# Optimization experiments

Hardware: AMD Instinct MI355X
Metric: run time of the kernel (lower is better)

Reference implementation:

```python
import jax, jax.numpy as jnp
import numpy as np

S, N, MSA_DIM, PAIR_DIM, D, H = 8, 256, 256, 128, 32, 8
EPS = 1e-5


def layer_norm(x, w, b):
    mu = jnp.mean(x, axis=-1, keepdims=True)
    var = jnp.mean((x - mu) ** 2, axis=-1, keepdims=True)
    return (x - mu) * jax.lax.rsqrt(var + EPS) * w + b


def setup_inputs() -> dict:
    key = jax.random.key(0)
    ks = jax.random.split(key, 8)
    def rnd(k, shape, scale=1.0):
        return jax.random.normal(k, shape, jnp.float32) * scale
    return {
        "msa_rep": rnd(ks[0], (S, N, MSA_DIM)),
        "pair_rep": rnd(ks[1], (N, N, PAIR_DIM)),
        "ln_w": jnp.ones((MSA_DIM,), jnp.float32),
        "ln_b": jnp.zeros((MSA_DIM,), jnp.float32),
        "w_qkv": rnd(ks[2], (MSA_DIM, 3 * H * D), 0.02),
        "ln_pair_w": jnp.ones((PAIR_DIM,), jnp.float32),
        "ln_pair_b": jnp.zeros((PAIR_DIM,), jnp.float32),
        "w_b": rnd(ks[3], (PAIR_DIM, H), 0.02),
        "w_g": rnd(ks[4], (MSA_DIM, H * D), 0.02),
        "w_out": rnd(ks[5], (H * D, MSA_DIM), 0.02),
        "b_out": jnp.zeros((MSA_DIM,), jnp.float32),
    }


def reference(msa_rep, pair_rep, ln_w, ln_b, w_qkv, ln_pair_w, ln_pair_b,
              w_b, w_g, w_out, b_out):
    s, n, _ = msa_rep.shape
    x = layer_norm(msa_rep, ln_w, ln_b)                      # [s, n, msa_dim]
    qkv = x @ w_qkv                                          # [s, n, 3*h*d]
    # chunk(3, dim=-1) then view(..., d, h): d outer, h inner
    q, k, v = [t.reshape(s, n, D, H) for t in jnp.split(qkv, 3, axis=-1)]
    # pair bias: LN + linear -> [n, n, h], broadcast to [1, i, j, 1, h]
    b = layer_norm(pair_rep, ln_pair_w, ln_pair_b) @ w_b     # [n, n, h]
    g = jax.nn.sigmoid(x @ w_g).reshape(s, n, D, H)          # gate [s, n, d, h]
    # NOTE: logits keep the d axis (no contraction): einsum 'sidh,sjdh->sijdh'
    scores = (q[:, :, None, :, :] * k[:, None, :, :, :]) * (D ** -0.5) \
             + b[None, :, :, None, :]                        # [s, i, j, d, h]
    a = jax.nn.softmax(scores, axis=2)                       # softmax over j
    out = g * jnp.einsum('sijdh,sjdh->sidh', a, v)           # [s, n, d, h]
    return out.reshape(s, n, D * H) @ w_out + b_out          # [s, n, msa_dim]
```

## Files before the change

### kernel.cpp

```cpp
#include <hip/hip_runtime.h>
#include <math.h>

#define S_DIM 8
#define N_RES 256
#define MSA_DIM 256
#define PAIR_DIM 128
#define D_DIM 32
#define H_DIM 8
#define M_ROWS (S_DIM * N_RES)
#define QKV_N (3 * H_DIM * D_DIM)
#define HD (H_DIM * D_DIM)
#define LOG2E 1.4426950408889634f

#define DPP_ADD(x, ctrl, rmask)                                                \
    x += __int_as_float(__builtin_amdgcn_update_dpp(                           \
        0, __float_as_int(x), (ctrl), (rmask), 0xf, true))

__device__ __forceinline__ float wave_sum63(float x) {
    DPP_ADD(x, 0x111, 0xf);
    DPP_ADD(x, 0x112, 0xf);
    DPP_ADD(x, 0x114, 0xf);
    DPP_ADD(x, 0x118, 0xf);
    DPP_ADD(x, 0x142, 0xa);
    DPP_ADD(x, 0x143, 0xc);
    return x;
}

__device__ __forceinline__ float quad_sum(float x) {
    x += __int_as_float(__builtin_amdgcn_update_dpp(
        0, __float_as_int(x), 0xB1, 0xf, 0xf, true));
    x += __int_as_float(__builtin_amdgcn_update_dpp(
        0, __float_as_int(x), 0x4E, 0xf, 0xf, true));
    return x;
}

__global__ __launch_bounds__(256) void ln_msa_kernel(
    const float* __restrict__ msa, const float* __restrict__ w,
    const float* __restrict__ b, float* __restrict__ x)
{
    int row = blockIdx.x;
    int t = threadIdx.x;
    float v = msa[row * MSA_DIM + t];
    float s1 = wave_sum63(v);
    float s2 = wave_sum63(v * v);
    __shared__ float r1[4], r2[4];
    int wave = t >> 6, lane = t & 63;
    if (lane == 63) { r1[wave] = s1; r2[wave] = s2; }
    __syncthreads();
    float S1 = r1[0] + r1[1] + r1[2] + r1[3];
    float S2 = r2[0] + r2[1] + r2[2] + r2[3];
    float mu = S1 * (1.0f / 256.0f);
    float var = S2 * (1.0f / 256.0f) - mu * mu;
    float rs = rsqrtf(var + 1e-5f);
    x[row * MSA_DIM + t] = (v - mu) * rs * w[t] + b[t];
}

__global__ __launch_bounds__(256) void xw_kernel(
    const float* __restrict__ X, const float* __restrict__ Wqkv,
    const float* __restrict__ Wg, float* __restrict__ q_t,
    float* __restrict__ k_t, float* __restrict__ v_t, float* __restrict__ g_t)
{
    __shared__ float Xs[16][68];
    __shared__ float Ws[16][64];
    int t = threadIdx.x;
    int bx = blockIdx.x;
    int qkv_mode = (bx < 12);
    const float* W = qkv_mode ? Wqkv : Wg;
    int Ncols = qkv_mode ? QKV_N : HD;
    int n0 = qkv_mode ? bx * 64 : (bx - 12) * 64;
    int m0 = blockIdx.y * 64;
    int tm = t >> 4, tn = t & 15;
    int lxm = t >> 2, lxk = (t & 3) * 4;
    int lwk = t >> 4, lwn = (t & 15) * 4;
    float acc[4][4] = {};
    for (int k0 = 0; k0 < 256; k0 += 16) {
        float4 xa = *(const float4*)&X[(m0 + lxm) * 256 + k0 + lxk];
        float4 wa = *(const float4*)&W[(k0 + lwk) * Ncols + n0 + lwn];
        __syncthreads();
        Xs[lxk + 0][lxm] = xa.x; Xs[lxk + 1][lxm] = xa.y;
        Xs[lxk + 2][lxm] = xa.z; Xs[lxk + 3][lxm] = xa.w;
        *(float4*)&Ws[lwk][lwn] = wa;
        __syncthreads();
#pragma unroll
        for (int kk = 0; kk < 16; kk++) {
            float4 a4 = *(const float4*)&Xs[kk][tm * 4];
            float4 b4 = *(const float4*)&Ws[kk][tn * 4];
            acc[0][0] += a4.x * b4.x; acc[0][1] += a4.x * b4.y; acc[0][2] += a4.x * b4.z; acc[0][3] += a4.x * b4.w;
            acc[1][0] += a4.y * b4.x; acc[1][1] += a4.y * b4.y; acc[1][2] += a4.y * b4.z; acc[1][3] += a4.y * b4.w;
            acc[2][0] += a4.z * b4.x; acc[2][1] += a4.z * b4.y; acc[2][2] += a4.z * b4.z; acc[2][3] += a4.z * b4.w;
            acc[3][0] += a4.w * b4.x; acc[3][1] += a4.w * b4.y; acc[3][2] += a4.w * b4.z; acc[3][3] += a4.w * b4.w;
        }
    }
#pragma unroll
    for (int ii = 0; ii < 4; ii++) {
#pragma unroll
        for (int jj = 0; jj < 4; jj++) {
            float c = acc[ii][jj];
            int mm = m0 + tm * 4 + ii;
            int nn = n0 + tn * 4 + jj;
            if (qkv_mode) {
                int chunk = nn >> 8, r = nn & 255, d = r >> 3, h = r & 7;
                float* dst = (chunk == 0) ? q_t : ((chunk == 1) ? k_t : v_t);
                dst[(h * M_ROWS + mm) * D_DIM + d] = c;
            } else {
                int d = nn >> 3, h = nn & 7;
                g_t[(h * M_ROWS + mm) * D_DIM + d] = 1.0f / (1.0f + __expf(-c));
            }
        }
    }
}

__global__ __launch_bounds__(256) void out_gemm_kernel(
    const float* __restrict__ X, const float* __restrict__ W,
    const float* __restrict__ bias, float* __restrict__ out)
{
    __shared__ float Xs[16][68];
    __shared__ float Ws[16][64];
    int t = threadIdx.x;
    int m0 = blockIdx.y * 64, n0 = blockIdx.x * 64;
    int tm = t >> 4, tn = t & 15;
    int lxm = t >> 2, lxk = (t & 3) * 4;
    int lwk = t >> 4, lwn = (t & 15) * 4;
    float acc[4][4] = {};
    for (int k0 = 0; k0 < 256; k0 += 16) {
        int k = k0 + lwk;
        int wrow = (k & 31) * 8 + (k >> 5);
        float4 xa = *(const float4*)&X[(m0 + lxm) * 256 + k0 + lxk];
        float4 wa = *(const float4*)&W[wrow * 256 + n0 + lwn];
        __syncthreads();
        Xs[lxk + 0][lxm] = xa.x; Xs[lxk + 1][lxm] = xa.y;
        Xs[lxk + 2][lxm] = xa.z; Xs[lxk + 3][lxm] = xa.w;
        *(float4*)&Ws[lwk][lwn] = wa;
        __syncthreads();
#pragma unroll
        for (int kk = 0; kk < 16; kk++) {
            float4 a4 = *(const float4*)&Xs[kk][tm * 4];
            float4 b4 = *(const float4*)&Ws[kk][tn * 4];
            acc[0][0] += a4.x * b4.x; acc[0][1] += a4.x * b4.y; acc[0][2] += a4.x * b4.z; acc[0][3] += a4.x * b4.w;
            acc[1][0] += a4.y * b4.x; acc[1][1] += a4.y * b4.y; acc[1][2] += a4.y * b4.z; acc[1][3] += a4.y * b4.w;
            acc[2][0] += a4.z * b4.x; acc[2][1] += a4.z * b4.y; acc[2][2] += a4.z * b4.z; acc[2][3] += a4.z * b4.w;
            acc[3][0] += a4.w * b4.x; acc[3][1] += a4.w * b4.y; acc[3][2] += a4.w * b4.z; acc[3][3] += a4.w * b4.w;
        }
    }
#pragma unroll
    for (int ii = 0; ii < 4; ii++) {
#pragma unroll
        for (int jj = 0; jj < 4; jj++) {
            int mm = m0 + tm * 4 + ii;
            int nn = n0 + tn * 4 + jj;
            out[mm * 256 + nn] = acc[ii][jj] + bias[nn];
        }
    }
}

__global__ __launch_bounds__(128) void pb_setup_kernel(
    const float* __restrict__ lw, const float* __restrict__ lb,
    const float* __restrict__ wb, float* __restrict__ Abuf)
{
    __shared__ float P[128][8], Q[128][8];
    int c = threadIdx.x;
    float lwc = lw[c], lbc = lb[c];
#pragma unroll
    for (int h = 0; h < 8; h++) {
        float w = wb[c * 8 + h];
        float a = lwc * w;
        P[c][h] = a;
        Q[c][h] = lbc * w;
        Abuf[c * 12 + h] = a * LOG2E;
    }
    __syncthreads();
    if (c < 8) {
        float s = 0, cc = 0;
        for (int k = 0; k < 128; k++) { s += P[k][c]; cc += Q[k][c]; }
        Abuf[1536 + c] = s * LOG2E;
        Abuf[1544 + c] = cc * LOG2E;
    }
}

__global__ __launch_bounds__(256) void pair_bias_kernel(
    const float* __restrict__ pair, const float* __restrict__ Abuf,
    float* __restrict__ b2)
{
    __shared__ __align__(16) float As[1552];
    int t = threadIdx.x;
    for (int idx = t; idx < 388; idx += 256)
        ((float4*)As)[idx] = ((const float4*)Abuf)[idx];
    __syncthreads();
    int row = blockIdx.x * 64 + (t >> 2);
    int q = t & 3;
    const float* in = pair + (size_t)row * PAIR_DIM;
    float4 x4[8];
#pragma unroll
    for (int it = 0; it < 8; it++)
        x4[it] = *(const float4*)&in[it * 16 + q * 4];
    float s = 0, s2 = 0;
    float dot[8] = {};
#pragma unroll
    for (int it = 0; it < 8; it++) {
        float xk[4];
        *(float4*)xk = x4[it];
#pragma unroll
        for (int k = 0; k < 4; k++) {
            int c = it * 16 + q * 4 + k;
            float xv = xk[k];
            s += xv; s2 += xv * xv;
            float4 A0 = *(const float4*)&As[c * 12];
            float4 A1 = *(const float4*)&As[c * 12 + 4];
            dot[0] += xv * A0.x; dot[1] += xv * A0.y;
            dot[2] += xv * A0.z; dot[3] += xv * A0.w;
            dot[4] += xv * A1.x; dot[5] += xv * A1.y;
            dot[6] += xv * A1.z; dot[7] += xv * A1.w;
        }
    }
    s = quad_sum(s);
    s2 = quad_sum(s2);
#pragma unroll
    for (int h = 0; h < 8; h++) dot[h] = quad_sum(dot[h]);
    float mu = s * (1.0f / 128.0f);
    float var = s2 * (1.0f / 128.0f) - mu * mu;
    float rs = rsqrtf(var + 1e-5f);
    int h0 = q * 2;
#pragma unroll
    for (int u = 0; u < 2; u++) {
        int h = h0 + u;
        b2[h * 65536 + row] = rs * (dot[h] - mu * As[1536 + h]) + As[1544 + h];
    }
}

__global__ __launch_bounds__(256) void attn_kernel(
    const float* __restrict__ q_t, const float* __restrict__ k_t,
    const float* __restrict__ v_t, const float* __restrict__ g_t,
    const float* __restrict__ b2, float* __restrict__ ao)
{
    __shared__ float k_sh[256][32];
    __shared__ float v_sh[256][32];
    int blk = blockIdx.x;
    int s = blk >> 6, h = (blk >> 3) & 7, it = blk & 7;
    int t = threadIdx.x;
    const float* kb = k_t + (size_t)(h * M_ROWS + s * N_RES) * D_DIM;
    const float* vb = v_t + (size_t)(h * M_ROWS + s * N_RES) * D_DIM;
    for (int idx = t; idx < 2048; idx += 256) {
        ((float4*)k_sh)[idx] = ((const float4*)kb)[idx];
        ((float4*)v_sh)[idx] = ((const float4*)vb)[idx];
    }
    __syncthreads();
    int jp = t & 3, dg = (t >> 2) & 7, li = t >> 5;
    int d0 = dg * 4;
    const float SCL2 = 0.17677669529663687f * LOG2E;
    int ig[4], mrow[4];
    float qs[4][4];
#pragma unroll
    for (int r = 0; r < 4; r++) {
        ig[r] = it * 32 + r * 8 + li;
        mrow[r] = s * N_RES + ig[r];
        float4 q4 = *(const float4*)&q_t[(size_t)(h * M_ROWS + mrow[r]) * D_DIM + d0];
        qs[r][0] = q4.x * SCL2; qs[r][1] = q4.y * SCL2;
        qs[r][2] = q4.z * SCL2; qs[r][3] = q4.w * SCL2;
    }
    float den[4][4] = {}, acc[4][4] = {};
    const float* bbase = b2 + h * 65536;
    for (int js4 = 0; js4 < 16; js4++) {
        float bb[4][4];
#pragma unroll
        for (int r = 0; r < 4; r++)
            *(float4*)&bb[r][0] =
                *(const float4*)&bbase[ig[r] * 256 + jp * 64 + js4 * 4];
#pragma unroll
        for (int u = 0; u < 4; u++) {
            int j = jp * 64 + js4 * 4 + u;
            float ka[4], va[4];
            *(float4*)ka = *(const float4*)&k_sh[j][d0];
            *(float4*)va = *(const float4*)&v_sh[j][d0];
#pragma unroll
            for (int r = 0; r < 4; r++) {
#pragma unroll
                for (int c = 0; c < 4; c++) {
                    float e = __builtin_amdgcn_exp2f(qs[r][c] * ka[c] + bb[r][u]);
                    den[r][c] += e;
                    acc[r][c] += e * va[c];
                }
            }
        }
    }
#pragma unroll
    for (int r = 0; r < 4; r++)
#pragma unroll
        for (int c = 0; c < 4; c++) {
            den[r][c] = quad_sum(den[r][c]);
            acc[r][c] = quad_sum(acc[r][c]);
        }
    if (jp == 0) {
#pragma unroll
        for (int r = 0; r < 4; r++) {
            float4 g4 = *(const float4*)&g_t[(size_t)(h * M_ROWS + mrow[r]) * D_DIM + d0];
            float4 o;
            o.x = g4.x * acc[r][0] / den[r][0];
            o.y = g4.y * acc[r][1] / den[r][1];
            o.z = g4.z * acc[r][2] / den[r][2];
            o.w = g4.w * acc[r][3] / den[r][3];
            *(float4*)&ao[(size_t)mrow[r] * HD + h * 32 + d0] = o;
        }
    }
}

extern "C" void kernel_launch(void* const* d_in, const int* in_sizes, int n_in,
                              void* d_out, int out_size, void* d_ws, size_t ws_size,
                              hipStream_t stream)
{
    const float* msa_rep   = (const float*)d_in[0];
    const float* pair_rep  = (const float*)d_in[1];
    const float* ln_w      = (const float*)d_in[2];
    const float* ln_b      = (const float*)d_in[3];
    const float* w_qkv     = (const float*)d_in[4];
    const float* ln_pair_w = (const float*)d_in[5];
    const float* ln_pair_b = (const float*)d_in[6];
    const float* w_b       = (const float*)d_in[7];
    const float* w_g       = (const float*)d_in[8];
    const float* w_out     = (const float*)d_in[9];
    const float* b_out     = (const float*)d_in[10];
    float* out = (float*)d_out;

    float* ws = (float*)d_ws;
    const size_t CH = 524288;
    float* x    = ws + 0 * CH;
    float* q_t  = ws + 1 * CH;
    float* k_t  = ws + 2 * CH;
    float* v_t  = ws + 3 * CH;
    float* g_t  = ws + 4 * CH;
    float* b2   = ws + 5 * CH;
    float* ao   = ws + 6 * CH;
    float* Abuf = ws + 7 * CH;

    ln_msa_kernel<<<M_ROWS, 256, 0, stream>>>(msa_rep, ln_w, ln_b, x);

    xw_kernel<<<dim3(16, M_ROWS / 64), 256, 0, stream>>>(
        x, w_qkv, w_g, q_t, k_t, v_t, g_t);

    pb_setup_kernel<<<1, 128, 0, stream>>>(ln_pair_w, ln_pair_b, w_b, Abuf);

    pair_bias_kernel<<<65536 / 64, 256, 0, stream>>>(pair_rep, Abuf, b2);

    attn_kernel<<<512, 256, 0, stream>>>(q_t, k_t, v_t, g_t, b2, ao);

    out_gemm_kernel<<<dim3(HD / 64, M_ROWS / 64), 256, 0, stream>>>(
        ao, w_out, b_out, out);
}
```

Measured before the change: 170.4 us.

## Widen GEMM tiles, read weights directly from global, split-K output GEMM

Both projection GEMMs now use 64x128 tiles with a 4x8 register micro-tile and read weights directly from global/L2 instead of staging them in shared memory. The X tile load is software-prefetched one k-step ahead. The output GEMM is split-K into four partial buffers, with a new reduction kernel that adds the bias. The aim is more FMA work per shared load and more parallelism in the small output GEMM. The cost is extra partial-buffer traffic, one more kernel launch, and uncoalesced-per-k global weight loads that rely on cache hits.

```diff
diff --git a/kernel.cpp b/kernel.cpp
--- a/kernel.cpp
+++ b/kernel.cpp
@@ -61,49 +61,55 @@
     float* __restrict__ k_t, float* __restrict__ v_t, float* __restrict__ g_t)
 {
     __shared__ float Xs[16][68];
-    __shared__ float Ws[16][64];
     int t = threadIdx.x;
     int bx = blockIdx.x;
-    int qkv_mode = (bx < 12);
+    int qkv_mode = (bx < 6);
+    int n0 = bx * 128;
     const float* W = qkv_mode ? Wqkv : Wg;
     int Ncols = qkv_mode ? QKV_N : HD;
-    int n0 = qkv_mode ? bx * 64 : (bx - 12) * 64;
+    int wn0 = qkv_mode ? n0 : n0 - QKV_N;
     int m0 = blockIdx.y * 64;
     int tm = t >> 4, tn = t & 15;
     int lxm = t >> 2, lxk = (t & 3) * 4;
-    int lwk = t >> 4, lwn = (t & 15) * 4;
-    float acc[4][4] = {};
-    for (int k0 = 0; k0 < 256; k0 += 16) {
-        float4 xa = *(const float4*)&X[(m0 + lxm) * 256 + k0 + lxk];
-        float4 wa = *(const float4*)&W[(k0 + lwk) * Ncols + n0 + lwn];
+    const float* Wcol = W + wn0 + tn * 8;
+    float acc[4][8] = {};
+    float4 xa = *(const float4*)&X[(m0 + lxm) * 256 + lxk];
+    for (int kt = 0; kt < 16; kt++) {
         __syncthreads();
         Xs[lxk + 0][lxm] = xa.x; Xs[lxk + 1][lxm] = xa.y;
         Xs[lxk + 2][lxm] = xa.z; Xs[lxk + 3][lxm] = xa.w;
-        *(float4*)&Ws[lwk][lwn] = wa;
         __syncthreads();
+        if (kt < 15)
+            xa = *(const float4*)&X[(m0 + lxm) * 256 + (kt + 1) * 16 + lxk];
 #pragma unroll
         for (int kk = 0; kk < 16; kk++) {
-            float4 a4 = *(const float4*)&Xs[kk][tm * 4];
-            float4 b4 = *(const float4*)&Ws[kk][tn * 4];
-            acc[0][0] += a4.x * b4.x; acc[0][1] += a4.x * b4.y; acc[0][2] += a4.x * b4.z; acc[0][3] += a4.x * b4.w;
-            acc[1][0] += a4.y * b4.x; acc[1][1] += a4.y * b4.y; acc[1][2] += a4.y * b4.z; acc[1][3] += a4.y * b4.w;
-            acc[2][0] += a4.z * b4.x; acc[2][1] += a4.z * b4.y; acc[2][2] += a4.z * b4.z; acc[2][3] += a4.z * b4.w;
-            acc[3][0] += a4.w * b4.x; acc[3][1] += a4.w * b4.y; acc[3][2] += a4.w * b4.z; acc[3][3] += a4.w * b4.w;
-        }
-    }
-#pragma unroll
-    for (int ii = 0; ii < 4; ii++) {
-#pragma unroll
-        for (int jj = 0; jj < 4; jj++) {
-            float c = acc[ii][jj];
-            int mm = m0 + tm * 4 + ii;
-            int nn = n0 + tn * 4 + jj;
+            float a[4];
+            *(float4*)a = *(const float4*)&Xs[kk][tm * 4];
+            const float* wr = Wcol + (size_t)(kt * 16 + kk) * Ncols;
+            float b[8];
+            *(float4*)&b[0] = *(const float4*)&wr[0];
+            *(float4*)&b[4] = *(const float4*)&wr[4];
+#pragma unroll
+            for (int i = 0; i < 4; i++)
+#pragma unroll
+                for (int u = 0; u < 8; u++) acc[i][u] += a[i] * b[u];
+        }
+    }
+    int nbase = n0 + tn * 8;
+#pragma unroll
+    for (int i = 0; i < 4; i++) {
+        int mm = m0 + tm * 4 + i;
+#pragma unroll
+        for (int u = 0; u < 8; u++) {
+            float c = acc[i][u];
+            int nn = nbase + u;
             if (qkv_mode) {
                 int chunk = nn >> 8, r = nn & 255, d = r >> 3, h = r & 7;
                 float* dst = (chunk == 0) ? q_t : ((chunk == 1) ? k_t : v_t);
                 dst[(h * M_ROWS + mm) * D_DIM + d] = c;
             } else {
-                int d = nn >> 3, h = nn & 7;
+                int gn = nn - QKV_N;
+                int d = gn >> 3, h = gn & 7;
                 g_t[(h * M_ROWS + mm) * D_DIM + d] = 1.0f / (1.0f + __expf(-c));
             }
         }
@@ -112,45 +118,68 @@
 
 __global__ __launch_bounds__(256) void out_gemm_kernel(
     const float* __restrict__ X, const float* __restrict__ W,
-    const float* __restrict__ bias, float* __restrict__ out)
+    float* __restrict__ part)
 {
     __shared__ float Xs[16][68];
-    __shared__ float Ws[16][64];
-    int t = threadIdx.x;
-    int m0 = blockIdx.y * 64, n0 = blockIdx.x * 64;
+    int t = threadIdx.x;
+    int n0 = blockIdx.x * 128;
+    int m0 = blockIdx.y * 64;
+    int k0g = blockIdx.z * 64;
     int tm = t >> 4, tn = t & 15;
     int lxm = t >> 2, lxk = (t & 3) * 4;
-    int lwk = t >> 4, lwn = (t & 15) * 4;
-    float acc[4][4] = {};
-    for (int k0 = 0; k0 < 256; k0 += 16) {
-        int k = k0 + lwk;
-        int wrow = (k & 31) * 8 + (k >> 5);
-        float4 xa = *(const float4*)&X[(m0 + lxm) * 256 + k0 + lxk];
-        float4 wa = *(const float4*)&W[wrow * 256 + n0 + lwn];
+    const float* Wcol = W + n0 + tn * 8;
+    float acc[4][8] = {};
+    float4 xa = *(const float4*)&X[(m0 + lxm) * 256 + k0g + lxk];
+    for (int kt = 0; kt < 4; kt++) {
         __syncthreads();
         Xs[lxk + 0][lxm] = xa.x; Xs[lxk + 1][lxm] = xa.y;
         Xs[lxk + 2][lxm] = xa.z; Xs[lxk + 3][lxm] = xa.w;
-        *(float4*)&Ws[lwk][lwn] = wa;
         __syncthreads();
+        if (kt < 3)
+            xa = *(const float4*)&X[(m0 + lxm) * 256 + k0g + (kt + 1) * 16 + lxk];
 #pragma unroll
         for (int kk = 0; kk < 16; kk++) {
-            float4 a4 = *(const float4*)&Xs[kk][tm * 4];
-            float4 b4 = *(const float4*)&Ws[kk][tn * 4];
-            acc[0][0] += a4.x * b4.x; acc[0][1] += a4.x * b4.y; acc[0][2] += a4.x * b4.z; acc[0][3] += a4.x * b4.w;
-            acc[1][0] += a4.y * b4.x; acc[1][1] += a4.y * b4.y; acc[1][2] += a4.y * b4.z; acc[1][3] += a4.y * b4.w;
-            acc[2][0] += a4.z * b4.x; acc[2][1] += a4.z * b4.y; acc[2][2] += a4.z * b4.z; acc[2][3] += a4.z * b4.w;
-            acc[3][0] += a4.w * b4.x; acc[3][1] += a4.w * b4.y; acc[3][2] += a4.w * b4.z; acc[3][3] += a4.w * b4.w;
-        }
-    }
-#pragma unroll
-    for (int ii = 0; ii < 4; ii++) {
-#pragma unroll
-        for (int jj = 0; jj < 4; jj++) {
-            int mm = m0 + tm * 4 + ii;
-            int nn = n0 + tn * 4 + jj;
-            out[mm * 256 + nn] = acc[ii][jj] + bias[nn];
-        }
-    }
+            int k = k0g + kt * 16 + kk;
+            int wrow = (k & 31) * 8 + (k >> 5);
+            float a[4];
+            *(float4*)a = *(const float4*)&Xs[kk][tm * 4];
+            const float* wr = Wcol + (size_t)wrow * 256;
+            float b[8];
+            *(float4*)&b[0] = *(const float4*)&wr[0];
+            *(float4*)&b[4] = *(const float4*)&wr[4];
+#pragma unroll
+            for (int i = 0; i < 4; i++)
+#pragma unroll
+                for (int u = 0; u < 8; u++) acc[i][u] += a[i] * b[u];
+        }
+    }
+    float* pb = part + (size_t)blockIdx.z * (M_ROWS * 256);
+#pragma unroll
+    for (int i = 0; i < 4; i++) {
+        int mm = m0 + tm * 4 + i;
+        *(float4*)&pb[mm * 256 + n0 + tn * 8] = *(float4*)&acc[i][0];
+        *(float4*)&pb[mm * 256 + n0 + tn * 8 + 4] = *(float4*)&acc[i][4];
+    }
+}
+
+__global__ __launch_bounds__(256) void reduce_out_kernel(
+    const float* __restrict__ part, const float* __restrict__ bias,
+    float* __restrict__ out)
+{
+    int idx = blockIdx.x * 256 + threadIdx.x;
+    int e = idx * 4;
+    int n = e & 255;
+    float4 p0 = *(const float4*)&part[e];
+    float4 p1 = *(const float4*)&part[e + M_ROWS * 256];
+    float4 p2 = *(const float4*)&part[e + 2 * M_ROWS * 256];
+    float4 p3 = *(const float4*)&part[e + 3 * M_ROWS * 256];
+    float4 bb = *(const float4*)&bias[n];
+    float4 o;
+    o.x = p0.x + p1.x + p2.x + p3.x + bb.x;
+    o.y = p0.y + p1.y + p2.y + p3.y + bb.y;
+    o.z = p0.z + p1.z + p2.z + p3.z + bb.z;
+    o.w = p0.w + p1.w + p2.w + p3.w + bb.w;
+    *(float4*)&out[e] = o;
 }
 
 __global__ __launch_bounds__(128) void pb_setup_kernel(
@@ -330,10 +359,11 @@
     float* b2   = ws + 5 * CH;
     float* ao   = ws + 6 * CH;
     float* Abuf = ws + 7 * CH;
+    float* part = ws + 8 * CH;
 
     ln_msa_kernel<<<M_ROWS, 256, 0, stream>>>(msa_rep, ln_w, ln_b, x);
 
-    xw_kernel<<<dim3(16, M_ROWS / 64), 256, 0, stream>>>(
+    xw_kernel<<<dim3(8, 32), 256, 0, stream>>>(
         x, w_qkv, w_g, q_t, k_t, v_t, g_t);
 
     pb_setup_kernel<<<1, 128, 0, stream>>>(ln_pair_w, ln_pair_b, w_b, Abuf);
@@ -342,6 +372,7 @@
 
     attn_kernel<<<512, 256, 0, stream>>>(q_t, k_t, v_t, g_t, b2, ao);
 
-    out_gemm_kernel<<<dim3(HD / 64, M_ROWS / 64), 256, 0, stream>>>(
-        ao, w_out, b_out, out);
-}
+    out_gemm_kernel<<<dim3(2, 32, 4), 256, 0, stream>>>(ao, w_out, part);
+
+    reduce_out_kernel<<<512, 256, 0, stream>>>(part, b_out, out);
+}
```

Result: slower. 191.1 us (+12.1%).
